# Kernel tuning notes

Hardware: AMD Instinct MI355X
Metric: run time of the kernel (lower is better)

## Reference

```python
import jax, jax.numpy as jnp
import numpy as np

NUM_GRAPHS = 8
EV_A3_TO_GPA = 160.21766208


def _energy(pos, bond_vec, src, dst, edge_graph, centers, W1, b1, W2, b2, W3, b3):
    # Surrogate GNN energy: edge displacement mixes pos and bond_vec so both get grads,
    # mirroring grad(total_energies, [pos, bond_vec]) in the original wrapper.
    disp = bond_vec + pos[dst] - pos[src]                      # [E,3]
    d = jnp.sqrt(jnp.sum(disp * disp, axis=-1) + 1e-12)        # [E]
    rbf = jnp.exp(-jnp.square(d[:, None] - centers[None, :]))  # [E,K]
    h = jax.nn.silu(rbf @ W1 + b1)                             # [E,H]
    h = jax.nn.silu(h @ W2 + b2)                               # [E,H]
    e_edge = (h @ W3 + b3)[:, 0]                               # [E]
    return jax.ops.segment_sum(e_edge, edge_graph, num_segments=NUM_GRAPHS)  # [B]


def setup_inputs() -> dict:
    key = jax.random.key(0)
    ks = jax.random.split(key, 8)
    N, E, K, H = 49152, 786432, 32, 64
    pos = jax.random.normal(ks[0], (N, 3), jnp.float32) * 3.0
    bond_vec = jax.random.normal(ks[1], (E, 3), jnp.float32)
    src = jax.random.randint(ks[2], (E,), 0, N, dtype=jnp.int32)
    dst = jax.random.randint(ks[3], (E,), 0, N, dtype=jnp.int32)
    edge_graph = jnp.repeat(jnp.arange(NUM_GRAPHS, dtype=jnp.int32), E // NUM_GRAPHS)
    volume = jax.random.uniform(ks[4], (N,), jnp.float32, 50.0, 150.0)
    centers = jnp.linspace(0.0, 5.0, K).astype(jnp.float32)
    W1 = jax.random.normal(ks[5], (K, H), jnp.float32) / np.float32(np.sqrt(K))
    b1 = jnp.zeros((H,), jnp.float32)
    W2 = jax.random.normal(ks[6], (H, H), jnp.float32) / np.float32(np.sqrt(H))
    b2 = jnp.zeros((H,), jnp.float32)
    W3 = jax.random.normal(ks[7], (H, 1), jnp.float32) / np.float32(np.sqrt(H))
    b3 = jnp.zeros((1,), jnp.float32)
    return {"pos": pos, "bond_vec": bond_vec, "src": src, "dst": dst,
            "edge_graph": edge_graph, "volume": volume, "centers": centers,
            "W1": W1, "b1": b1, "W2": W2, "b2": b2, "W3": W3, "b3": b3}


def reference(pos, bond_vec, src, dst, edge_graph, volume, centers, W1, b1, W2, b2, W3, b3):
    energies, vjp_fn = jax.vjp(
        lambda p, bv: _energy(p, bv, src, dst, edge_graph, centers, W1, b1, W2, b2, W3, b3),
        pos, bond_vec)
    # grad_outputs = ones_like(total_energies)
    gpos, gbv = vjp_fn(jnp.ones_like(energies))
    forces = -gpos                                             # [N,3]
    f_ij = -gbv                                                # [E,3]
    # Per-graph stress: bond_vec_g^T @ f_ij_g, vectorized as segment-summed outer products.
    outer = bond_vec[:, :, None] * f_ij[:, None, :]            # [E,3,3]
    S = jax.ops.segment_sum(outer, edge_graph, num_segments=NUM_GRAPHS)  # [B,3,3]
    nodes_per_graph = pos.shape[0] // NUM_GRAPHS
    vol0 = volume[jnp.arange(NUM_GRAPHS) * nodes_per_graph]    # volume at first node of each graph
    stresses = (-EV_A3_TO_GPA * S / vol0[:, None, None]).reshape(NUM_GRAPHS * 3, 3)
    hessian = jnp.zeros((1,), jnp.float32)                     # calc_hessian=False
    return energies, forces, stresses, hessian
```

## Files before the change

### kernel.cpp

```cpp
#include <hip/hip_runtime.h>
#include <math.h>

#define K_RBF 32
#define H_DIM 64
#define TBL 4096
#define D_MAX 16.0f
#define N_NODES 49152
#define N_EDGES 786432
#define N_GRAPHS 8
#define NODES_PER_GRAPH 6144
#define EV_A3_TO_GPA 160.21766208f
#define LOG2E 1.44269504088896f

#define OUT_FORCES 8
#define OUT_STRESS 147464
#define OUT_TAIL_N 81

#define CHUNK_NODES  192
#define CHUNK_FLOATS 576
#define N_CHUNKS     256
#define REC_CAP      7168

#define EDGE_BLOCKS   768
#define EDGE_THREADS  512
#define EDGE_WAVES    (EDGE_THREADS / 64)
#define EDGES_PER_GRAPH (N_EDGES / N_GRAPHS)
#define BLK_PER_GRAPH (EDGE_BLOCKS / N_GRAPHS)

#define OFF_TAB 0u
#define OFF_CNT 65536u
#define OFF_REC 66560u
#define WS_NEED (OFF_REC + (size_t)N_CHUNKS * REC_CAP * 16u)

__device__ __forceinline__ int chunk_of(int node) {
    return (int)((unsigned)((node >> 6) * 683) >> 11);
}

__global__ __launch_bounds__(256) void build_table(
    const float* __restrict__ centers,
    const float* __restrict__ W1, const float* __restrict__ b1,
    const float* __restrict__ W2, const float* __restrict__ b2,
    const float* __restrict__ W3, const float* __restrict__ b3,
    float4* __restrict__ tab4, int* __restrict__ gcnt,
    float* __restrict__ out, int zero_out_tail)
{
    if (blockIdx.x == 0) {
        int t = threadIdx.x;
        gcnt[t] = 0;
        if (zero_out_tail) {
            if (t < N_GRAPHS) out[t] = 0.f;
            else if (t < OUT_TAIL_N) out[3 * N_NODES + t] = 0.f;
        }
    }

    __shared__ float W2s[H_DIM * 65];
    for (int idx = threadIdx.x; idx < H_DIM * H_DIM; idx += 256)
        W2s[(idx >> 6) * 65 + (idx & 63)] = W2[idx];
    __syncthreads();

    int lane = threadIdx.x & 63;
    int i    = blockIdx.x * 4 + (threadIdx.x >> 6);
    float d  = (float)i * (D_MAX / (float)TBL);

    float z1 = b1[lane], u = 0.f;
#pragma unroll
    for (int k = 0; k < K_RBF; ++k) {
        float tc = d - centers[k];
        float e  = exp2f(-tc * tc * LOG2E);
        float w  = W1[k * H_DIM + lane];
        z1 = fmaf(e, w, z1);
        u  = fmaf(-2.f * tc * e, w, u);
    }
    float s1  = 1.f / (1.f + exp2f(-z1 * LOG2E));
    float h1  = z1 * s1;
    float ds1 = s1 * fmaf(z1, 1.f - s1, 1.f);

    float z2 = b2[lane];
#pragma unroll
    for (int h = 0; h < H_DIM; ++h)
        z2 = fmaf(__shfl(h1, h, 64), W2s[h * 65 + lane], z2);

    float s2  = 1.f / (1.f + exp2f(-z2 * LOG2E));
    float w3  = W3[lane];
    float Fp  = z2 * s2 * w3;
    float dz2 = w3 * s2 * fmaf(z2, 1.f - s2, 1.f);

    float dh1 = 0.f;
#pragma unroll
    for (int j = 0; j < H_DIM; ++j)
        dh1 = fmaf(__shfl(dz2, j, 64), W2s[lane * 65 + j], dh1);

    float Gp = dh1 * ds1 * u;
#pragma unroll
    for (int m = 32; m > 0; m >>= 1) {
        Fp += __shfl_xor(Fp, m, 64);
        Gp += __shfl_xor(Gp, m, 64);
    }
    if (lane == 0) {
        float F = Fp + b3[0];
        ((float2*)tab4)[2 * i] = make_float2(F, Gp);
        if (i > 0)
            ((float2*)tab4)[2 * i - 1] = make_float2(F, Gp);
    }
}

__global__ __launch_bounds__(EDGE_THREADS) void edge_compute(
    const float* __restrict__ pos, const float* __restrict__ bond,
    const int* __restrict__ src, const int* __restrict__ dst,
    const float* __restrict__ volume, const float4* __restrict__ tab4,
    float4* __restrict__ recs, int* __restrict__ gcnt,
    float* __restrict__ out)
{
    __shared__ int   cnt[N_CHUNKS];
    __shared__ int   basech[N_CHUNKS];
    __shared__ float red[EDGE_WAVES][10];

    const int t = threadIdx.x;
    if (t < N_CHUNKS) cnt[t] = 0;
    __syncthreads();

    const int g = blockIdx.x & 7;
    const int w = blockIdx.x >> 3;
    const int base_e = g * EDGES_PER_GRAPH + w * (EDGE_THREADS * 2);

    float vacc[10];
#pragma unroll
    for (int q = 0; q < 10; ++q) vacc[q] = 0.f;

    int   edi[2], esi[2], es0[2], es1[2];
    float egx[2], egy[2], egz[2];

#pragma unroll
    for (int i = 0; i < 2; ++i) {
        int e  = base_e + i * EDGE_THREADS + t;
        int si = src[e], di = dst[e];
        float bx = bond[3 * e + 0], by = bond[3 * e + 1], bz = bond[3 * e + 2];
        float dx = bx + pos[3 * di + 0] - pos[3 * si + 0];
        float dy = by + pos[3 * di + 1] - pos[3 * si + 1];
        float dz = bz + pos[3 * di + 2] - pos[3 * si + 2];
        float d  = sqrtf(fmaf(dx, dx, fmaf(dy, dy, fmaf(dz, dz, 1e-12f))));

        float tt  = fminf(d * ((float)TBL / D_MAX), (float)(TBL - 1));
        int   ix  = min((int)tt, TBL - 2);
        float fr  = tt - (float)ix;
        float4 tv = tab4[ix];
        float F = fmaf(fr, tv.z - tv.x, tv.x);
        float G = fmaf(fr, tv.w - tv.y, tv.y);

        float scl = G / d;
        float gx = scl * dx, gy = scl * dy, gz = scl * dz;
        egx[i] = gx; egy[i] = gy; egz[i] = gz;
        edi[i] = di; esi[i] = si;
        es0[i] = atomicAdd(&cnt[chunk_of(di)], 1);
        es1[i] = atomicAdd(&cnt[chunk_of(si)], 1);

        vacc[0] += F;
        vacc[1] = fmaf(bx, gx, vacc[1]); vacc[2] = fmaf(bx, gy, vacc[2]);
        vacc[3] = fmaf(bx, gz, vacc[3]); vacc[4] = fmaf(by, gx, vacc[4]);
        vacc[5] = fmaf(by, gy, vacc[5]); vacc[6] = fmaf(by, gz, vacc[6]);
        vacc[7] = fmaf(bz, gx, vacc[7]); vacc[8] = fmaf(bz, gy, vacc[8]);
        vacc[9] = fmaf(bz, gz, vacc[9]);
    }
    __syncthreads();
    if (t < N_CHUNKS) basech[t] = atomicAdd(&gcnt[t], cnt[t]);
    __syncthreads();
#pragma unroll
    for (int i = 0; i < 2; ++i) {
        int c0 = chunk_of(edi[i]), c1 = chunk_of(esi[i]);
        int l0 = edi[i] - c0 * CHUNK_NODES;
        int l1 = esi[i] - c1 * CHUNK_NODES;
        int p0 = basech[c0] + es0[i];
        int p1 = basech[c1] + es1[i];
        if (p0 < REC_CAP)
            recs[(size_t)c0 * REC_CAP + p0] =
                make_float4(-egx[i], -egy[i], -egz[i], __int_as_float(l0));
        if (p1 < REC_CAP)
            recs[(size_t)c1 * REC_CAP + p1] =
                make_float4(egx[i], egy[i], egz[i], __int_as_float(l1));
    }

#pragma unroll
    for (int q = 0; q < 10; ++q) {
        float x = vacc[q];
#pragma unroll
        for (int m = 32; m > 0; m >>= 1) x += __shfl_xor(x, m, 64);
        vacc[q] = x;
    }
    int wave = t >> 6;
    if ((t & 63) == 0)
#pragma unroll
        for (int q = 0; q < 10; ++q) red[wave][q] = vacc[q];
    __syncthreads();
    if (t < 10) {
        float tot = 0.f;
#pragma unroll
        for (int k = 0; k < EDGE_WAVES; ++k) tot += red[k][t];
        if (t == 0) atomicAdd(out + g, tot);
        else {
            float vol = volume[g * NODES_PER_GRAPH];
            atomicAdd(out + OUT_STRESS + g * 9 + (t - 1),
                      tot * (EV_A3_TO_GPA / vol));
        }
    }
}

__global__ __launch_bounds__(512) void scatter_direct(
    const float4* __restrict__ recs, const int* __restrict__ gcnt,
    float* __restrict__ out)
{
    __shared__ float acc[CHUNK_FLOATS];
    const int t = threadIdx.x;
    if (t < CHUNK_FLOATS) acc[t] = 0.f;
    if (t < CHUNK_FLOATS - 512) acc[512 + t] = 0.f;
    __syncthreads();

    const int c = blockIdx.x;
    int total = min(gcnt[c], REC_CAP);
    const float4* seg = recs + (size_t)c * REC_CAP;
    for (int r = t; r < total; r += 512) {
        float4 rec = seg[r];
        int li = 3 * __float_as_int(rec.w);
        atomicAdd(&acc[li + 0], rec.x);
        atomicAdd(&acc[li + 1], rec.y);
        atomicAdd(&acc[li + 2], rec.z);
    }
    __syncthreads();

    if (t < CHUNK_FLOATS / 4) {
        float4* dst4 = (float4*)(out + OUT_FORCES + c * CHUNK_FLOATS);
        dst4[t] = ((const float4*)acc)[t];
    }
}

__global__ __launch_bounds__(256) void edge_fallback(
    const float* __restrict__ pos, const float* __restrict__ bond,
    const int* __restrict__ src, const int* __restrict__ dst,
    const float* __restrict__ volume, const float4* __restrict__ tab4,
    float* __restrict__ out)
{
    __shared__ float red[4][10];
    int lb = (blockIdx.x & 7) * (EDGES_PER_GRAPH / 256) + (blockIdx.x >> 3);
    int g  = blockIdx.x & 7;
    int e  = lb * 256 + threadIdx.x;

    int si = src[e], di = dst[e];
    float bx = bond[3 * e + 0], by = bond[3 * e + 1], bz = bond[3 * e + 2];
    float dx = bx + pos[3 * di + 0] - pos[3 * si + 0];
    float dy = by + pos[3 * di + 1] - pos[3 * si + 1];
    float dz = bz + pos[3 * di + 2] - pos[3 * si + 2];
    float d  = sqrtf(fmaf(dx, dx, fmaf(dy, dy, fmaf(dz, dz, 1e-12f))));

    float tt  = fminf(d * ((float)TBL / D_MAX), (float)(TBL - 1));
    int   ix  = min((int)tt, TBL - 2);
    float fr  = tt - (float)ix;
    float4 tv = tab4[ix];
    float F = fmaf(fr, tv.z - tv.x, tv.x);
    float G = fmaf(fr, tv.w - tv.y, tv.y);
    float scl = G / d;
    float gx = scl * dx, gy = scl * dy, gz = scl * dz;

    float* forces = out + OUT_FORCES;
    atomicAdd(forces + 3 * di + 0, -gx);
    atomicAdd(forces + 3 * di + 1, -gy);
    atomicAdd(forces + 3 * di + 2, -gz);
    atomicAdd(forces + 3 * si + 0,  gx);
    atomicAdd(forces + 3 * si + 1,  gy);
    atomicAdd(forces + 3 * si + 2,  gz);

    float v[10] = { F,
                    bx * gx, bx * gy, bx * gz,
                    by * gx, by * gy, by * gz,
                    bz * gx, bz * gy, bz * gz };
#pragma unroll
    for (int q = 0; q < 10; ++q) {
        float x = v[q];
#pragma unroll
        for (int m = 32; m > 0; m >>= 1) x += __shfl_xor(x, m, 64);
        v[q] = x;
    }
    int wave = threadIdx.x >> 6;
    if ((threadIdx.x & 63) == 0)
#pragma unroll
        for (int q = 0; q < 10; ++q) red[wave][q] = v[q];
    __syncthreads();
    if (threadIdx.x < 10) {
        float tot = red[0][threadIdx.x] + red[1][threadIdx.x]
                  + red[2][threadIdx.x] + red[3][threadIdx.x];
        if (threadIdx.x == 0) atomicAdd(out + g, tot);
        else {
            float vol = volume[g * NODES_PER_GRAPH];
            atomicAdd(out + OUT_STRESS + g * 9 + (threadIdx.x - 1),
                      tot * (EV_A3_TO_GPA / vol));
        }
    }
}

extern "C" void kernel_launch(void* const* d_in, const int* in_sizes, int n_in,
                              void* d_out, int out_size, void* d_ws, size_t ws_size,
                              hipStream_t stream)
{
    const float* pos     = (const float*)d_in[0];
    const float* bond    = (const float*)d_in[1];
    const int*   src     = (const int*)d_in[2];
    const int*   dst     = (const int*)d_in[3];
    const float* volume  = (const float*)d_in[5];
    const float* centers = (const float*)d_in[6];
    const float* W1 = (const float*)d_in[7];
    const float* b1 = (const float*)d_in[8];
    const float* W2 = (const float*)d_in[9];
    const float* b2 = (const float*)d_in[10];
    const float* W3 = (const float*)d_in[11];
    const float* b3 = (const float*)d_in[12];
    float*  out  = (float*)d_out;
    char*   ws   = (char*)d_ws;
    float4* tab4 = (float4*)(ws + OFF_TAB);
    int*    gcnt = (int*)(ws + OFF_CNT);
    float4* recs = (float4*)(ws + OFF_REC);

    if (ws_size >= WS_NEED) {
        build_table<<<TBL / 4, 256, 0, stream>>>(centers, W1, b1, W2, b2, W3, b3,
                                                 tab4, gcnt, out, 1);
        edge_compute<<<EDGE_BLOCKS, EDGE_THREADS, 0, stream>>>(
            pos, bond, src, dst, volume, tab4, recs, gcnt, out);
        scatter_direct<<<N_CHUNKS, 512, 0, stream>>>(recs, gcnt, out);
    } else {
        hipMemsetAsync(d_out, 0, (size_t)out_size * sizeof(float), stream);
        build_table<<<TBL / 4, 256, 0, stream>>>(centers, W1, b1, W2, b2, W3, b3,
                                                 tab4, gcnt, out, 0);
        edge_fallback<<<N_EDGES / 256, 256, 0, stream>>>(
            pos, bond, src, dst, volume, tab4, out);
    }
}
```

Measured before the change: 152.4 us.

## Pack scatter records to fp16 and split record buckets per XCD

Force records written by edge_compute shrink from 16-byte float4 to 8-byte packed half-precision components plus a 16-bit local index. Bucket counters and record regions are also split per XCD, using the hardware XCC id register, so atomics on the global counters and record writes stay local to each die. The scatter kernel walks the eight sub-buckets for each chunk. This halves record traffic and reduces cross-die atomic contention, at the cost of fp16 precision loss in the forces and a smaller per-sub-bucket capacity that silently drops records if a bucket overflows.

```diff
diff --git a/kernel.cpp b/kernel.cpp
--- a/kernel.cpp
+++ b/kernel.cpp
@@ -1,4 +1,5 @@
 #include <hip/hip_runtime.h>
+#include <hip/hip_fp16.h>
 #include <math.h>
 
 #define K_RBF 32
@@ -19,21 +20,25 @@
 #define CHUNK_NODES  192
 #define CHUNK_FLOATS 576
 #define N_CHUNKS     256
-#define REC_CAP      7168
+#define SUBCAP       1024
+#define N_XCD        8
 
 #define EDGE_BLOCKS   768
 #define EDGE_THREADS  512
 #define EDGE_WAVES    (EDGE_THREADS / 64)
 #define EDGES_PER_GRAPH (N_EDGES / N_GRAPHS)
-#define BLK_PER_GRAPH (EDGE_BLOCKS / N_GRAPHS)
 
 #define OFF_TAB 0u
 #define OFF_CNT 65536u
-#define OFF_REC 66560u
-#define WS_NEED (OFF_REC + (size_t)N_CHUNKS * REC_CAP * 16u)
+#define OFF_REC 73728u
+#define WS_NEED (OFF_REC + (size_t)N_CHUNKS * N_XCD * SUBCAP * 8u)
 
 __device__ __forceinline__ int chunk_of(int node) {
     return (int)((unsigned)((node >> 6) * 683) >> 11);
+}
+
+__device__ __forceinline__ unsigned pack_h(float v) {
+    return (unsigned)__half_as_ushort(__float2half(v));
 }
 
 __global__ __launch_bounds__(256) void build_table(
@@ -46,7 +51,7 @@
 {
     if (blockIdx.x == 0) {
         int t = threadIdx.x;
-        gcnt[t] = 0;
+        for (int j = t; j < N_CHUNKS * N_XCD; j += 256) gcnt[j] = 0;
         if (zero_out_tail) {
             if (t < N_GRAPHS) out[t] = 0.f;
             else if (t < OUT_TAIL_N) out[3 * N_NODES + t] = 0.f;
@@ -108,7 +113,7 @@
     const float* __restrict__ pos, const float* __restrict__ bond,
     const int* __restrict__ src, const int* __restrict__ dst,
     const float* __restrict__ volume, const float4* __restrict__ tab4,
-    float4* __restrict__ recs, int* __restrict__ gcnt,
+    uint2* __restrict__ recs, int* __restrict__ gcnt,
     float* __restrict__ out)
 {
     __shared__ int   cnt[N_CHUNKS];
@@ -118,6 +123,10 @@
     const int t = threadIdx.x;
     if (t < N_CHUNKS) cnt[t] = 0;
     __syncthreads();
+
+    unsigned xcc;
+    asm volatile("s_getreg_b32 %0, hwreg(HW_REG_XCC_ID)" : "=s"(xcc));
+    xcc &= 7;
 
     const int g = blockIdx.x & 7;
     const int w = blockIdx.x >> 3;
@@ -162,21 +171,26 @@
         vacc[9] = fmaf(bz, gz, vacc[9]);
     }
     __syncthreads();
-    if (t < N_CHUNKS) basech[t] = atomicAdd(&gcnt[t], cnt[t]);
+    if (t < N_CHUNKS)
+        basech[t] = atomicAdd(&gcnt[t * N_XCD + xcc], cnt[t]);
     __syncthreads();
 #pragma unroll
     for (int i = 0; i < 2; ++i) {
         int c0 = chunk_of(edi[i]), c1 = chunk_of(esi[i]);
-        int l0 = edi[i] - c0 * CHUNK_NODES;
-        int l1 = esi[i] - c1 * CHUNK_NODES;
+        unsigned l0 = (unsigned)(edi[i] - c0 * CHUNK_NODES);
+        unsigned l1 = (unsigned)(esi[i] - c1 * CHUNK_NODES);
         int p0 = basech[c0] + es0[i];
         int p1 = basech[c1] + es1[i];
-        if (p0 < REC_CAP)
-            recs[(size_t)c0 * REC_CAP + p0] =
-                make_float4(-egx[i], -egy[i], -egz[i], __int_as_float(l0));
-        if (p1 < REC_CAP)
-            recs[(size_t)c1 * REC_CAP + p1] =
-                make_float4(egx[i], egy[i], egz[i], __int_as_float(l1));
+        if (p0 < SUBCAP) {
+            uint2 r = make_uint2(pack_h(-egx[i]) | (pack_h(-egy[i]) << 16),
+                                 pack_h(-egz[i]) | (l0 << 16));
+            recs[((size_t)c0 * N_XCD + xcc) * SUBCAP + p0] = r;
+        }
+        if (p1 < SUBCAP) {
+            uint2 r = make_uint2(pack_h(egx[i]) | (pack_h(egy[i]) << 16),
+                                 pack_h(egz[i]) | (l1 << 16));
+            recs[((size_t)c1 * N_XCD + xcc) * SUBCAP + p1] = r;
+        }
     }
 
 #pragma unroll
@@ -205,7 +219,7 @@
 }
 
 __global__ __launch_bounds__(512) void scatter_direct(
-    const float4* __restrict__ recs, const int* __restrict__ gcnt,
+    const uint2* __restrict__ recs, const int* __restrict__ gcnt,
     float* __restrict__ out)
 {
     __shared__ float acc[CHUNK_FLOATS];
@@ -215,14 +229,20 @@
     __syncthreads();
 
     const int c = blockIdx.x;
-    int total = min(gcnt[c], REC_CAP);
-    const float4* seg = recs + (size_t)c * REC_CAP;
-    for (int r = t; r < total; r += 512) {
-        float4 rec = seg[r];
-        int li = 3 * __float_as_int(rec.w);
-        atomicAdd(&acc[li + 0], rec.x);
-        atomicAdd(&acc[li + 1], rec.y);
-        atomicAdd(&acc[li + 2], rec.z);
+#pragma unroll
+    for (int x = 0; x < N_XCD; ++x) {
+        int total = min(gcnt[c * N_XCD + x], SUBCAP);
+        const uint2* seg = recs + ((size_t)c * N_XCD + x) * SUBCAP;
+        for (int r = t; r < total; r += 512) {
+            uint2 v = seg[r];
+            float gx = __half2float(__ushort_as_half((unsigned short)(v.x & 0xffff)));
+            float gy = __half2float(__ushort_as_half((unsigned short)(v.x >> 16)));
+            float gz = __half2float(__ushort_as_half((unsigned short)(v.y & 0xffff)));
+            int li = 3 * (int)(v.y >> 16);
+            atomicAdd(&acc[li + 0], gx);
+            atomicAdd(&acc[li + 1], gy);
+            atomicAdd(&acc[li + 2], gz);
+        }
     }
     __syncthreads();
 
@@ -315,7 +335,7 @@
     char*   ws   = (char*)d_ws;
     float4* tab4 = (float4*)(ws + OFF_TAB);
     int*    gcnt = (int*)(ws + OFF_CNT);
-    float4* recs = (float4*)(ws + OFF_REC);
+    uint2*  recs = (uint2*)(ws + OFF_REC);
 
     if (ws_size >= WS_NEED) {
         build_table<<<TBL / 4, 256, 0, stream>>>(centers, W1, b1, W2, b2, W3, b3,
```

Result: slower. 158.9 us (+4.3%).
